# Performance work log

Measured on AMD Instinct MI355X. Metric: run time of the kernel, lower is better.

Reference implementation:

```python
import jax, jax.numpy as jnp
import numpy as np

B, S, H, OUT = 64, 513, 1024, 128   # batch, seq (incl CLS), hidden, slot labels
T = S - 1                            # subword tokens after dropping [CLS]
P_WORD_START = 0.75                  # avg ~1.33 subwords per word


def setup_inputs() -> dict:
    key = jax.random.key(0)
    k1, k2, k3, k4 = jax.random.split(key, 4)
    hidden_states = jax.random.normal(k1, (B, S, H), jnp.float32)
    W = jax.random.normal(k2, (H, OUT), jnp.float32) * 0.02
    b = jax.random.normal(k3, (OUT,), jnp.float32) * 0.02
    # contiguous, non-decreasing word ids: cumsum of word-start flags
    starts = (jax.random.uniform(k4, (B, T)) < P_WORD_START).astype(jnp.int32)
    starts = starts.at[:, 0].set(1)
    segment_ids = jnp.cumsum(starts, axis=-1) - 1  # [B, T], values in [0, n_words)
    return {"hidden_states": hidden_states, "W": W, "b": b,
            "segment_ids": segment_ids}


def _merge_row(logits, seg):
    # logits: [T, OUT], seg: [T] contiguous non-decreasing word ids
    s = jax.ops.segment_sum(logits, seg, num_segments=T)                    # [T, OUT]
    c = jax.ops.segment_sum(jnp.ones((T,), logits.dtype), seg, num_segments=T)
    mean = s / jnp.maximum(c, 1.0)[:, None]
    # words beyond n_words (empty segments) -> zero padding, as in the original
    return jnp.where(c[:, None] > 0, mean, 0.0)


def reference(hidden_states, W, b, segment_ids):
    x = hidden_states[:, 1:]                       # drop [CLS]; dropout = identity (eval)
    logits = jnp.einsum('bth,ho->bto', x, W) + b   # [B, T, OUT]
    merged = jax.vmap(_merge_row)(logits, segment_ids)  # per-word ragged mean + pad
    return jnp.transpose(merged, (0, 2, 1))        # [B, OUT, T]
```

## Files before the change

### kernel.cpp

```cpp
#include <hip/hip_runtime.h>
#include <hip/hip_bf16.h>

#define B_    64
#define S_    513
#define T_    512
#define H_    1024
#define OUT_  128

#define BM 64
#define BN 128
#define BK 32
#define NKT (H_ / BK)

typedef __attribute__((ext_vector_type(8))) short short8_t;
typedef __attribute__((ext_vector_type(4))) float f32x4;

__device__ inline ushort f2bf(float f) {
    union { float f; unsigned u; } x; x.f = f;
    unsigned r = x.u + 0x7fffu + ((x.u >> 16) & 1u);
    return (ushort)(r >> 16);
}

__global__ __launch_bounds__(256) void wt_kernel(
    const float* __restrict__ W, ushort* __restrict__ Wt)
{
    __shared__ ushort tile[64][65];
    int k0 = blockIdx.x * 64, o0 = blockIdx.y * 64;
    int tid = threadIdx.x;
#pragma unroll
    for (int p = 0; p < 16; ++p) {
        int idx = tid + p * 256;
        int r = idx >> 6, c = idx & 63;
        tile[r][c] = f2bf(W[(size_t)(k0 + r) * OUT_ + o0 + c]);
    }
    __syncthreads();
#pragma unroll
    for (int p = 0; p < 16; ++p) {
        int idx = tid + p * 256;
        int c = idx >> 6, r = idx & 63;
        Wt[(size_t)(o0 + c) * H_ + k0 + r] = tile[r][c];
    }
}

__global__ __launch_bounds__(T_) void seg_info_kernel(
    const int* __restrict__ seg, int* __restrict__ seg_start,
    int* __restrict__ seg_cnt)
{
    int b = blockIdx.x;
    int t = threadIdx.x;
    __shared__ int s_start[T_];
    __shared__ int s_cnt[T_];
    s_start[t] = T_;
    s_cnt[t]   = 0;
    __syncthreads();
    int sid = seg[b * T_ + t];
    atomicMin(&s_start[sid], t);
    atomicAdd(&s_cnt[sid], 1);
    __syncthreads();
    seg_start[b * T_ + t] = s_start[t];
    seg_cnt[b * T_ + t]   = s_cnt[t];
}

__global__ __launch_bounds__(256) void gemm_kernel(
    const float* __restrict__ hs, const ushort* __restrict__ Wt,
    const float* __restrict__ bias, float* __restrict__ logits)
{
    __shared__ __align__(16) ushort As[2][BM * BK];
    __shared__ __align__(16) ushort Bs[2][BN * BK];

    int blk = blockIdx.x;
    int b   = blk >> 3;
    int t0  = (blk & 7) * BM;
    int tid = threadIdx.x;
    int lane = tid & 63;
    int wv = tid >> 6;
    int wm = wv & 1, wn = wv >> 1;
    int l15 = lane & 15, ksl = lane >> 4;

    int rowA = tid >> 2;
    int cblk = tid & 3;
    int rowB1 = rowA + 64;

    const float*  aptr  = hs + ((size_t)(b * S_ + 1 + t0) + rowA) * H_ + cblk * 8;
    const ushort* bptr0 = Wt + (size_t)rowA  * H_ + cblk * 8;
    const ushort* bptr1 = Wt + (size_t)rowB1 * H_ + cblk * 8;

    auto swz = [](int row, int blkc) {
        return row * BK + ((blkc ^ ((row >> 1) & 3)) << 3);
    };
    int wAo  = swz(rowA, cblk);
    int wB0o = swz(rowA, cblk);
    int wB1o = swz(rowB1, cblk);

    int rAo[2], rBo[4];
#pragma unroll
    for (int fm = 0; fm < 2; ++fm) {
        int row = wm * 32 + fm * 16 + l15;
        rAo[fm] = swz(row, ksl);
    }
#pragma unroll
    for (int fn = 0; fn < 4; ++fn) {
        int row = wn * 64 + fn * 16 + l15;
        rBo[fn] = swz(row, ksl);
    }

    f32x4 acc[2][4];
#pragma unroll
    for (int fm = 0; fm < 2; ++fm)
#pragma unroll
        for (int fn = 0; fn < 4; ++fn) acc[fm][fn] = (f32x4){0.f, 0.f, 0.f, 0.f};

    float4 ra0, ra1;
    int4 rb0, rb1;

    auto loadT = [&](int kt) {
        const float* ap = aptr + kt * BK;
        ra0 = *reinterpret_cast<const float4*>(ap);
        ra1 = *reinterpret_cast<const float4*>(ap + 4);
        rb0 = *reinterpret_cast<const int4*>(bptr0 + kt * BK);
        rb1 = *reinterpret_cast<const int4*>(bptr1 + kt * BK);
    };
    auto writeT = [&](int nb) {
        union { ushort u[8]; int4 i; } pa;
        pa.u[0] = f2bf(ra0.x); pa.u[1] = f2bf(ra0.y);
        pa.u[2] = f2bf(ra0.z); pa.u[3] = f2bf(ra0.w);
        pa.u[4] = f2bf(ra1.x); pa.u[5] = f2bf(ra1.y);
        pa.u[6] = f2bf(ra1.z); pa.u[7] = f2bf(ra1.w);
        *reinterpret_cast<int4*>(&As[nb][wAo])  = pa.i;
        *reinterpret_cast<int4*>(&Bs[nb][wB0o]) = rb0;
        *reinterpret_cast<int4*>(&Bs[nb][wB1o]) = rb1;
    };
    auto computeT = [&](int cb) {
        short8_t af[2], bf[4];
#pragma unroll
        for (int fm = 0; fm < 2; ++fm)
            af[fm] = *reinterpret_cast<const short8_t*>(&As[cb][rAo[fm]]);
#pragma unroll
        for (int fn = 0; fn < 4; ++fn)
            bf[fn] = *reinterpret_cast<const short8_t*>(&Bs[cb][rBo[fn]]);
#pragma unroll
        for (int fm = 0; fm < 2; ++fm)
#pragma unroll
            for (int fn = 0; fn < 4; ++fn)
                acc[fm][fn] = __builtin_amdgcn_mfma_f32_16x16x32_bf16(
                    af[fm], bf[fn], acc[fm][fn], 0, 0, 0);
    };

    loadT(0);
    writeT(0);
    __syncthreads();

    for (int kt = 0; kt < NKT; ++kt) {
        int cb = kt & 1;
        if (kt + 1 < NKT) loadT(kt + 1);
        computeT(cb);
        if (kt + 1 < NKT) writeT(cb ^ 1);
        __syncthreads();
    }

#pragma unroll
    for (int fn = 0; fn < 4; ++fn) {
        int o = wn * 64 + fn * 16 + l15;
        float bv = bias[o];
#pragma unroll
        for (int fm = 0; fm < 2; ++fm) {
#pragma unroll
            for (int r = 0; r < 4; ++r) {
                int t = t0 + wm * 32 + fm * 16 + ksl * 4 + r;
                logits[((size_t)b * T_ + t) * OUT_ + o] = acc[fm][fn][r] + bv;
            }
        }
    }
}

__global__ __launch_bounds__(256) void merge_kernel(
    const float* __restrict__ logits, const int* __restrict__ seg_start,
    const int* __restrict__ seg_cnt, float* __restrict__ out)
{
    int blk = blockIdx.x;
    int b   = blk >> 4;
    int s0  = (blk & 15) * 32;
    int tid = threadIdx.x;

    __shared__ float tile[OUT_][33];

#pragma unroll
    for (int it = 0; it < 16; ++it) {
        int idx = tid + it * 256;
        int sl  = idx >> 7;
        int o   = idx & 127;
        int s   = s0 + sl;
        int cnt = seg_cnt[b * T_ + s];
        float v = 0.f;
        if (cnt > 0) {
            int st = seg_start[b * T_ + s];
            float sum = 0.f;
            for (int i = 0; i < cnt; ++i)
                sum += logits[((size_t)b * T_ + st + i) * OUT_ + o];
            v = sum / (float)cnt;
        }
        tile[o][sl] = v;
    }
    __syncthreads();

#pragma unroll
    for (int p = 0; p < 16; ++p) {
        int o  = (tid >> 5) + p * 8;
        int sl = tid & 31;
        out[((size_t)b * OUT_ + o) * T_ + s0 + sl] = tile[o][sl];
    }
}

extern "C" void kernel_launch(void* const* d_in, const int* in_sizes, int n_in,
                              void* d_out, int out_size, void* d_ws, size_t ws_size,
                              hipStream_t stream) {
    const float* hs   = (const float*)d_in[0];
    const float* W    = (const float*)d_in[1];
    const float* bias = (const float*)d_in[2];
    const int*   seg  = (const int*)d_in[3];
    float* out = (float*)d_out;

    float* logits    = (float*)d_ws;
    int*   seg_start = (int*)((char*)d_ws + (size_t)B_ * T_ * OUT_ * sizeof(float));
    int*   seg_cnt   = seg_start + (size_t)B_ * T_;
    ushort* Wt       = (ushort*)(seg_cnt + (size_t)B_ * T_);

    wt_kernel<<<dim3(H_ / 64, OUT_ / 64), 256, 0, stream>>>(W, Wt);
    seg_info_kernel<<<B_, T_, 0, stream>>>(seg, seg_start, seg_cnt);
    gemm_kernel<<<B_ * (T_ / BM), 256, 0, stream>>>(hs, Wt, bias, logits);
    merge_kernel<<<B_ * (T_ / 32), 256, 0, stream>>>(logits, seg_start, seg_cnt, out);
}
```

Before: 56.75 us.

## Fuse segment-info into merge kernel, store bf16 logits, move bias to merge

```diff
diff --git a/kernel.cpp b/kernel.cpp
--- a/kernel.cpp
+++ b/kernel.cpp
@@ -19,6 +19,9 @@
     union { float f; unsigned u; } x; x.f = f;
     unsigned r = x.u + 0x7fffu + ((x.u >> 16) & 1u);
     return (ushort)(r >> 16);
+}
+__device__ inline float bf2f(ushort u) {
+    union { unsigned u; float f; } x; x.u = (unsigned)u << 16; return x.f;
 }
 
 __global__ __launch_bounds__(256) void wt_kernel(
@@ -42,28 +45,9 @@
     }
 }
 
-__global__ __launch_bounds__(T_) void seg_info_kernel(
-    const int* __restrict__ seg, int* __restrict__ seg_start,
-    int* __restrict__ seg_cnt)
-{
-    int b = blockIdx.x;
-    int t = threadIdx.x;
-    __shared__ int s_start[T_];
-    __shared__ int s_cnt[T_];
-    s_start[t] = T_;
-    s_cnt[t]   = 0;
-    __syncthreads();
-    int sid = seg[b * T_ + t];
-    atomicMin(&s_start[sid], t);
-    atomicAdd(&s_cnt[sid], 1);
-    __syncthreads();
-    seg_start[b * T_ + t] = s_start[t];
-    seg_cnt[b * T_ + t]   = s_cnt[t];
-}
-
 __global__ __launch_bounds__(256) void gemm_kernel(
     const float* __restrict__ hs, const ushort* __restrict__ Wt,
-    const float* __restrict__ bias, float* __restrict__ logits)
+    ushort* __restrict__ logits)
 {
     __shared__ __align__(16) ushort As[2][BM * BK];
     __shared__ __align__(16) ushort Bs[2][BN * BK];
@@ -161,52 +145,65 @@
 #pragma unroll
     for (int fn = 0; fn < 4; ++fn) {
         int o = wn * 64 + fn * 16 + l15;
-        float bv = bias[o];
 #pragma unroll
         for (int fm = 0; fm < 2; ++fm) {
 #pragma unroll
             for (int r = 0; r < 4; ++r) {
                 int t = t0 + wm * 32 + fm * 16 + ksl * 4 + r;
-                logits[((size_t)b * T_ + t) * OUT_ + o] = acc[fm][fn][r] + bv;
+                logits[((size_t)b * T_ + t) * OUT_ + o] = f2bf(acc[fm][fn][r]);
             }
         }
     }
 }
 
 __global__ __launch_bounds__(256) void merge_kernel(
-    const float* __restrict__ logits, const int* __restrict__ seg_start,
-    const int* __restrict__ seg_cnt, float* __restrict__ out)
+    const ushort* __restrict__ logits, const int* __restrict__ seg,
+    const float* __restrict__ bias, float* __restrict__ out)
 {
     int blk = blockIdx.x;
-    int b   = blk >> 4;
-    int s0  = (blk & 15) * 32;
+    int b   = blk >> 3;
+    int s0  = (blk & 7) * 64;
     int tid = threadIdx.x;
 
-    __shared__ float tile[OUT_][33];
-
-#pragma unroll
-    for (int it = 0; it < 16; ++it) {
+    __shared__ int   sstart[64];
+    __shared__ int   scnt[64];
+    __shared__ float tile[OUT_][65];
+
+    if (tid < 64) { sstart[tid] = T_; scnt[tid] = 0; }
+    __syncthreads();
+#pragma unroll
+    for (int p = 0; p < 2; ++p) {
+        int t = tid + p * 256;
+        int li = seg[b * T_ + t] - s0;
+        if (li >= 0 && li < 64) {
+            atomicMin(&sstart[li], t);
+            atomicAdd(&scnt[li], 1);
+        }
+    }
+    __syncthreads();
+
+#pragma unroll
+    for (int it = 0; it < 32; ++it) {
         int idx = tid + it * 256;
         int sl  = idx >> 7;
         int o   = idx & 127;
-        int s   = s0 + sl;
-        int cnt = seg_cnt[b * T_ + s];
+        int c   = scnt[sl];
         float v = 0.f;
-        if (cnt > 0) {
-            int st = seg_start[b * T_ + s];
+        if (c > 0) {
+            int st = sstart[sl];
+            const ushort* src = logits + ((size_t)b * T_ + st) * OUT_ + o;
             float sum = 0.f;
-            for (int i = 0; i < cnt; ++i)
-                sum += logits[((size_t)b * T_ + st + i) * OUT_ + o];
-            v = sum / (float)cnt;
+            for (int i = 0; i < c; ++i) sum += bf2f(src[(size_t)i * OUT_]);
+            v = sum / (float)c + bias[o];
         }
         tile[o][sl] = v;
     }
     __syncthreads();
 
 #pragma unroll
-    for (int p = 0; p < 16; ++p) {
-        int o  = (tid >> 5) + p * 8;
-        int sl = tid & 31;
+    for (int p = 0; p < 32; ++p) {
+        int o  = (tid >> 6) + p * 4;
+        int sl = tid & 63;
         out[((size_t)b * OUT_ + o) * T_ + s0 + sl] = tile[o][sl];
     }
 }
@@ -220,13 +217,10 @@
     const int*   seg  = (const int*)d_in[3];
     float* out = (float*)d_out;
 
-    float* logits    = (float*)d_ws;
-    int*   seg_start = (int*)((char*)d_ws + (size_t)B_ * T_ * OUT_ * sizeof(float));
-    int*   seg_cnt   = seg_start + (size_t)B_ * T_;
-    ushort* Wt       = (ushort*)(seg_cnt + (size_t)B_ * T_);
+    ushort* logits = (ushort*)d_ws;
+    ushort* Wt     = logits + (size_t)B_ * T_ * OUT_;
 
     wt_kernel<<<dim3(H_ / 64, OUT_ / 64), 256, 0, stream>>>(W, Wt);
-    seg_info_kernel<<<B_, T_, 0, stream>>>(seg, seg_start, seg_cnt);
-    gemm_kernel<<<B_ * (T_ / BM), 256, 0, stream>>>(hs, Wt, bias, logits);
-    merge_kernel<<<B_ * (T_ / 32), 256, 0, stream>>>(logits, seg_start, seg_cnt, out);
-}
+    gemm_kernel<<<B_ * (T_ / BM), 256, 0, stream>>>(hs, Wt, logits);
+    merge_kernel<<<B_ * (T_ / 64), 256, 0, stream>>>(logits, seg, bias, out);
+}
```

New measurement: 57.33 us, median of 2. About the same (+1.0%).
